# Performance work log

Measured on AMD Instinct MI355X. Metric: run time of the kernel, lower is better.

Reference implementation:

```python
import jax, jax.numpy as jnp
import numpy as np

N = 50000   # nodes
E = 800000  # edges
F = 128     # input features
W = 128     # hidden width
K = 5       # Chebyshev order


def setup_inputs() -> dict:
    key = jax.random.key(0)
    ks = jax.random.split(key, 12)
    x = jax.random.normal(ks[0], (N, F), jnp.float32)
    edge_index = jax.random.randint(ks[1], (2, E), 0, N, jnp.int32)
    def p(i, shape):
        return jax.random.normal(ks[i], shape, jnp.float32) * 0.05
    return {
        'x': x,
        'edge_index': edge_index,
        'W0': p(2, (K, F, W)), 'b0': p(3, (W,)),
        'W1': p(4, (K, W, W)), 'b1': p(5, (W,)),
        'W2': p(6, (K, W, W)), 'b2': p(7, (W,)),
        'Wl': p(8, (W, 1)),   'bl': p(9, (1,)),
    }


def _norm(edge_index):
    # PyG ChebConv norm with lambda_max=2.0, sym normalization:
    # Lhat = 2/lambda_max * (I - D^-1/2 A D^-1/2) - I  ->  diag 0, offdiag -d_r*d_c
    src, dst = edge_index[0], edge_index[1]
    ew = (src != dst).astype(jnp.float32)  # remove self loops
    deg = jax.ops.segment_sum(ew, src, num_segments=N)
    dinv = jnp.where(deg > 0, jax.lax.rsqrt(jnp.maximum(deg, 1.0)), 0.0)
    w = -ew * dinv[src] * dinv[dst]
    return src, dst, w


def _cheb_conv(h, Wk, b, src, dst, w):
    # Tx_0 = h; Tx_1 = Lhat h; Tx_k = 2 Lhat Tx_{k-1} - Tx_{k-2}
    def matvec(v):
        # gather from src, weight, scatter-add to dst: [E, C] message tensor
        return jax.ops.segment_sum(w[:, None] * v[src], dst, num_segments=N)
    Tx0 = h
    out = Tx0 @ Wk[0]
    Tx1 = matvec(Tx0)
    out = out + Tx1 @ Wk[1]
    for k in range(2, Wk.shape[0]):
        Tx2 = 2.0 * matvec(Tx1) - Tx0
        out = out + Tx2 @ Wk[k]
        Tx0, Tx1 = Tx1, Tx2
    return out + b


def reference(x, edge_index, W0, b0, W1, b1, W2, b2, Wl, bl):
    src, dst, w = _norm(edge_index)
    h = jax.nn.relu(_cheb_conv(x, W0, b0, src, dst, w))  # dropout = identity (eval)
    h = jax.nn.relu(_cheb_conv(h, W1, b1, src, dst, w))
    h = _cheb_conv(h, W2, b2, src, dst, w)
    return h @ Wl + bl  # [N, 1]
```

## Files before the change

kernel.cpp:

```cpp
#include <hip/hip_runtime.h>
#include <hip/hip_bf16.h>
#include <stdint.h>

#define N_NODES 50000
#define N_EDGES 800000
#define FEAT 128
#define CAP 64
#define NCVT 1600000

#define B_CONV 6250
#define B_TRW  640
#define B_EDGE 3125
#define B_TOT  10018

typedef __attribute__((ext_vector_type(4))) float floatx4;
typedef __attribute__((ext_vector_type(8))) _Float16 half8;
typedef __attribute__((ext_vector_type(4))) _Float16 half4;
typedef __attribute__((ext_vector_type(4))) unsigned short ushortx4;

__device__ __forceinline__ float bf2f(unsigned short u) {
  union { unsigned u; float f; } v; v.u = ((unsigned)u) << 16; return v.f;
}
__device__ __forceinline__ unsigned short f2bf(float f) {
  union { float f; unsigned u; } v; v.f = f;
  unsigned r = v.u + 0x7fffu + ((v.u >> 16) & 1u);
  return (unsigned short)(r >> 16);
}
__device__ __forceinline__ unsigned pack_edge(float w, int s) {
  _Float16 h = (_Float16)w;
  unsigned short hb = __builtin_bit_cast(unsigned short, h);
  return ((unsigned)s << 16) | (unsigned)hb;
}
__device__ __forceinline__ float edge_w(unsigned e) {
  unsigned short hb = (unsigned short)(e & 0xFFFFu);
  return (float)__builtin_bit_cast(_Float16, hb);
}
__device__ __forceinline__ int edge_src(unsigned e) { return (int)(e >> 16); }

__global__ void k_pre1(const unsigned short* __restrict__ x,
                       const void* b0, const void* b1, const void* b2,
                       const void* wl, const void* bl,
                       float* __restrict__ pf, int* __restrict__ flag) {
  __shared__ int cnt_s;
  __shared__ int fl_s;
  int tid = threadIdx.x;
  if (tid == 0) cnt_s = 0;
  __syncthreads();
  int big = 0;
  for (int i = tid; i < 4096; i += 256) {
    unsigned short u = x[2 * i];
    int e = (u >> 7) & 0xFF;
    if (e >= 0xE0) big++;
  }
  atomicAdd(&cnt_s, big);
  __syncthreads();
  if (tid == 0) { fl_s = (cnt_s > 16) ? 1 : 0; flag[0] = fl_s; }
  __syncthreads();
  int fl = fl_s;
  for (int i = tid; i < 513; i += 256) {
    const void* src; int off;
    if (i < 128)      { src = b0; off = i; }
    else if (i < 256) { src = b1; off = i - 128; }
    else if (i < 384) { src = b2; off = i - 256; }
    else if (i < 512) { src = wl; off = i - 384; }
    else              { src = bl; off = 0; }
    pf[i] = fl ? ((const float*)src)[off] : bf2f(((const unsigned short*)src)[off]);
  }
}

__global__ void k_pre2(const void* __restrict__ xp,
                       const void* __restrict__ w0, const void* __restrict__ w1,
                       const void* __restrict__ w2,
                       const int* __restrict__ esrc, const int* __restrict__ edst,
                       _Float16* __restrict__ t0,
                       unsigned char* __restrict__ q0, float* __restrict__ s0,
                       _Float16* __restrict__ wt,
                       int* __restrict__ deg, int* __restrict__ cnt,
                       unsigned short* __restrict__ edata16,
                       float* __restrict__ pf,
                       const int* __restrict__ flag) {
  int b = blockIdx.x, tid = threadIdx.x;
  int o;
  if (b < 10000) {
    int g = b >> 4, r = b & 15;
    if (r < 5) {
      int e = (g * 5 + r) * 256 + tid;
      int s = __builtin_nontemporal_load(esrc + e);
      int d = __builtin_nontemporal_load(edst + e);
      if (s == d) return;
      atomicAdd(&deg[s], 1);
      int pos = atomicAdd(&cnt[d], 1);
      if (pos < CAP) edata16[((size_t)d << 6) + pos] = (unsigned short)s;
      return;
    }
    o = g * 11 + (r - 5);
  } else {
    o = 6875 + (b - 10000);
  }
  if (o < B_CONV) {
    int i = o * 256 + tid;
    int fl = flag[0];
    floatx4 v;
    if (fl) {
      v = __builtin_nontemporal_load((const floatx4*)xp + i);
    } else {
      ushortx4 u = __builtin_nontemporal_load((const ushortx4*)xp + i);
      v.x = bf2f(u.x); v.y = bf2f(u.y); v.z = bf2f(u.z); v.w = bf2f(u.w);
    }
    half4 h;
    h[0] = (_Float16)v.x; h[1] = (_Float16)v.y; h[2] = (_Float16)v.z; h[3] = (_Float16)v.w;
    ((half4*)t0)[i] = h;
    float mx = fmaxf(fmaxf(fabsf(v.x), fabsf(v.y)), fmaxf(fabsf(v.z), fabsf(v.w)));
#pragma unroll
    for (int d = 1; d < 32; d <<= 1) mx = fmaxf(mx, __shfl_xor(mx, d));
    float inv = mx > 0.f ? 127.f / mx : 0.f;
    int qa = (int)rintf(v.x * inv) + 128;
    int qb = (int)rintf(v.y * inv) + 128;
    int qc = (int)rintf(v.z * inv) + 128;
    int qd = (int)rintf(v.w * inv) + 128;
    ((unsigned*)q0)[i] = (unsigned)qa | ((unsigned)qb << 8) | ((unsigned)qc << 16) | ((unsigned)qd << 24);
    if ((i & 31) == 0) s0[i >> 5] = mx > 0.f ? mx / 127.f : 0.f;
  } else if (o < B_CONV + B_TRW) {
    int t = (o - B_CONV) * 256 + tid;
    int fl = flag[0];
    int li = t >> 14;
    int r = t & 16383;
    int n = r >> 7, kk = r & 127;
    int l = li / 5, k = li - l * 5;
    const void* w = (l == 0) ? w0 : w1;
    int idx = k * 16384 + kk * 128 + n;
    float v = fl ? ((const float*)w)[idx] : bf2f(((const unsigned short*)w)[idx]);
    wt[t] = (_Float16)v;
  } else {
    int t = (o - B_CONV - B_TRW) * 256 + tid;
    if (t > 640) return;
    int fl = flag[0];
    if (t < 640) {
      int k = t >> 7, f = t & 127;
      float s = 0.f;
      const int base = (k << 14) + (f << 7);
      if (fl) {
        const float* w = (const float*)w2 + base;
#pragma unroll 8
        for (int q = 0; q < 128; ++q) s += w[q] * pf[384 + q];
      } else {
        const unsigned short* w = (const unsigned short*)w2 + base;
#pragma unroll 8
        for (int q = 0; q < 128; ++q) s += bf2f(w[q]) * pf[384 + q];
      }
      pf[520 + t] = s;
    } else {
      float s = 0.f;
      for (int q = 0; q < 128; ++q) s += pf[256 + q] * pf[384 + q];
      pf[1160] = s + pf[512];
    }
  }
}

__global__ __launch_bounds__(256) void k_wpack(const unsigned short* __restrict__ ed16,
                                               const int* __restrict__ cnt,
                                               const int* __restrict__ deg,
                                               unsigned* __restrict__ edata) {
  int t = blockIdx.x * 256 + threadIdx.x;
  int node = t >> 6, slot = t & 63;
  if (node >= N_NODES) return;
  int n_e = cnt[node]; if (n_e > CAP) n_e = CAP;
  unsigned out = 0u;
  if (slot < n_e) {
    int s = (int)ed16[t];
    int dd = deg[node];
    int ds = deg[s];
    float w = (ds > 0 && dd > 0) ? -rsqrtf((float)ds) * rsqrtf((float)dd) : 0.f;
    out = pack_edge(w, s);
  }
  edata[t] = out;
}

__global__ __launch_bounds__(256) void k_spmv(const unsigned* __restrict__ edata,
                                              const int* __restrict__ cnt,
                                              const unsigned char* __restrict__ Q,
                                              const float* __restrict__ S,
                                              const _Float16* __restrict__ Z,
                                              _Float16* __restrict__ Y,
                                              unsigned char* __restrict__ Qo,
                                              float* __restrict__ So,
                                              float alpha, int hasZ, int wshadow) {
  int wave = threadIdx.x >> 6, lane = threadIdx.x & 63;
  int q = lane >> 4, l16 = lane & 15;
  int node = blockIdx.x * 16 + wave * 4 + q;
  if (node >= N_NODES) return;
  int n_e = cnt[node]; if (n_e > CAP) n_e = CAP;
  int base = node << 6;

  float acc[8];
#pragma unroll
  for (int f = 0; f < 8; ++f) acc[f] = 0.f;
  float wsum = 0.f;

  unsigned e0 = (0 < n_e) ? edata[base + 0] : 0u;
  unsigned e1 = (1 < n_e) ? edata[base + 1] : 0u;
  unsigned e2 = (2 < n_e) ? edata[base + 2] : 0u;
  unsigned e3 = (3 < n_e) ? edata[base + 3] : 0u;
  unsigned e4 = (4 < n_e) ? edata[base + 4] : 0u;
  unsigned e5 = (5 < n_e) ? edata[base + 5] : 0u;
  unsigned e6 = (6 < n_e) ? edata[base + 6] : 0u;
  unsigned e7 = (7 < n_e) ? edata[base + 7] : 0u;
  uint2 r0 = ((const uint2*)(Q + (size_t)edge_src(e0) * FEAT))[l16];
  uint2 r1 = ((const uint2*)(Q + (size_t)edge_src(e1) * FEAT))[l16];
  uint2 r2 = ((const uint2*)(Q + (size_t)edge_src(e2) * FEAT))[l16];
  uint2 r3 = ((const uint2*)(Q + (size_t)edge_src(e3) * FEAT))[l16];
  float s0 = S[edge_src(e0)], s1 = S[edge_src(e1)], s2 = S[edge_src(e2)], s3 = S[edge_src(e3)];

  for (int j = 0; j < n_e; j += 4) {
    float ws0 = edge_w(e0) * s0, ws1 = edge_w(e1) * s1;
    float ws2 = edge_w(e2) * s2, ws3 = edge_w(e3) * s3;
    uint2 c0 = r0, c1 = r1, c2 = r2, c3 = r3;
    e0 = e4; e1 = e5; e2 = e6; e3 = e7;
    e4 = (j + 8 < n_e) ? edata[base + j + 8] : 0u;
    e5 = (j + 9 < n_e) ? edata[base + j + 9] : 0u;
    e6 = (j + 10 < n_e) ? edata[base + j + 10] : 0u;
    e7 = (j + 11 < n_e) ? edata[base + j + 11] : 0u;
    r0 = ((const uint2*)(Q + (size_t)edge_src(e0) * FEAT))[l16];
    r1 = ((const uint2*)(Q + (size_t)edge_src(e1) * FEAT))[l16];
    r2 = ((const uint2*)(Q + (size_t)edge_src(e2) * FEAT))[l16];
    r3 = ((const uint2*)(Q + (size_t)edge_src(e3) * FEAT))[l16];
    s0 = S[edge_src(e0)]; s1 = S[edge_src(e1)]; s2 = S[edge_src(e2)]; s3 = S[edge_src(e3)];
#define DEC8(c, w)                                                        \
    acc[0] = fmaf(w, (float)(c.x & 0xFFu), acc[0]);                       \
    acc[1] = fmaf(w, (float)((c.x >> 8) & 0xFFu), acc[1]);                \
    acc[2] = fmaf(w, (float)((c.x >> 16) & 0xFFu), acc[2]);               \
    acc[3] = fmaf(w, (float)(c.x >> 24), acc[3]);                         \
    acc[4] = fmaf(w, (float)(c.y & 0xFFu), acc[4]);                       \
    acc[5] = fmaf(w, (float)((c.y >> 8) & 0xFFu), acc[5]);                \
    acc[6] = fmaf(w, (float)((c.y >> 16) & 0xFFu), acc[6]);               \
    acc[7] = fmaf(w, (float)(c.y >> 24), acc[7]);
    DEC8(c0, ws0) DEC8(c1, ws1) DEC8(c2, ws2) DEC8(c3, ws3)
#undef DEC8
    wsum += (ws0 + ws1) + (ws2 + ws3);
  }
  float rx[8];
  float b128 = 128.f * wsum;
  if (hasZ) {
    half8 z = ((const half8*)(Z + (size_t)node * FEAT))[l16];
#pragma unroll
    for (int f = 0; f < 8; ++f) rx[f] = fmaf(alpha, acc[f] - b128, -(float)z[f]);
  } else {
#pragma unroll
    for (int f = 0; f < 8; ++f) rx[f] = alpha * (acc[f] - b128);
  }
  half8 res;
#pragma unroll
  for (int f = 0; f < 8; ++f) res[f] = (_Float16)rx[f];
  ((half8*)(Y + (size_t)node * FEAT))[l16] = res;
  if (wshadow) {
    float mx = 0.f;
#pragma unroll
    for (int f = 0; f < 8; ++f) mx = fmaxf(mx, fabsf(rx[f]));
#pragma unroll
    for (int o = 1; o < 16; o <<= 1) mx = fmaxf(mx, __shfl_xor(mx, o));
    float inv = mx > 0.f ? 127.f / mx : 0.f;
    int qb[8];
#pragma unroll
    for (int f = 0; f < 8; ++f) qb[f] = (int)rintf(rx[f] * inv) + 128;
    uint2 p;
    p.x = (unsigned)qb[0] | ((unsigned)qb[1] << 8) | ((unsigned)qb[2] << 16) | ((unsigned)qb[3] << 24);
    p.y = (unsigned)qb[4] | ((unsigned)qb[5] << 8) | ((unsigned)qb[6] << 16) | ((unsigned)qb[7] << 24);
    ((uint2*)(Qo + (size_t)node * FEAT))[l16] = p;
    if (l16 == 0) So[node] = mx > 0.f ? mx / 127.f : 0.f;
  }
}

__global__ __launch_bounds__(256) void k_smv(const unsigned* __restrict__ edata,
                                             const int* __restrict__ cnt,
                                             const float* __restrict__ h,
                                             const float* __restrict__ b,
                                             const float* __restrict__ bprev,
                                             float cL, float* __restrict__ y,
                                             int is_out, void* __restrict__ outp,
                                             const int* __restrict__ flag,
                                             const float* __restrict__ cptr) {
  int wave = threadIdx.x >> 6, lane = threadIdx.x & 63;
  int q = lane >> 4, l16 = lane & 15;
  int node = blockIdx.x * 16 + wave * 4 + q;
  if (node >= N_NODES) return;
  int n_e = cnt[node]; if (n_e > CAP) n_e = CAP;
  int base = node << 6;
  float s = 0.f;
  for (int j = l16; j < n_e; j += 16) {
    unsigned e = edata[base + j];
    s = fmaf(edge_w(e), b[edge_src(e)], s);
  }
#pragma unroll
  for (int o = 1; o < 16; o <<= 1) s += __shfl_xor(s, o);
  if (l16 == 0) {
    float r = fmaf(cL, s, h[node]) - (bprev ? bprev[node] : 0.f);
    if (!is_out) {
      y[node] = r;
    } else {
      r += cptr[0];
      if (flag[0]) ((float*)outp)[node] = r;
      else ((unsigned short*)outp)[node] = f2bf(r);
    }
  }
}

__global__ __launch_bounds__(256) void k_gemm(const _Float16* __restrict__ t0, const _Float16* __restrict__ t1,
                                              const _Float16* __restrict__ t2, const _Float16* __restrict__ t3,
                                              const _Float16* __restrict__ t4,
                                              const _Float16* __restrict__ wt,
                                              const float* __restrict__ bias,
                                              _Float16* __restrict__ dst, int mode,
                                              const float* __restrict__ v0,
                                              float* __restrict__ hout,
                                              unsigned char* __restrict__ q8,
                                              float* __restrict__ sc) {
  __shared__ _Float16 lb[128 * 136];
  const _Float16* tp[5] = {t0, t1, t2, t3, t4};
  int tid = threadIdx.x, wave = tid >> 6, lane = tid & 63;
  int quad = lane >> 4, l16 = lane & 15;
  int m0 = blockIdx.x * 128;
  floatx4 acc[2][8];
#pragma unroll
  for (int s = 0; s < 2; ++s)
#pragma unroll
    for (int j = 0; j < 8; ++j) acc[s][j] = (floatx4){0.f, 0.f, 0.f, 0.f};
  int arow[2];
  bool aval[2];
#pragma unroll
  for (int s = 0; s < 2; ++s) {
    arow[s] = m0 + wave * 32 + s * 16 + l16;
    aval[s] = arow[s] < N_NODES;
  }

#pragma unroll
  for (int k = 0; k < 5; ++k) {
    __syncthreads();
    {
      int n = tid >> 1, half = tid & 1;
      const uint4* sp = (const uint4*)(wt + k * 16384 + n * 128 + half * 64);
      uint4* dq = (uint4*)(lb + n * 136 + half * 64);
#pragma unroll
      for (int i = 0; i < 8; ++i) dq[i] = sp[i];
    }
    __syncthreads();
    const _Float16* A = tp[k];
#pragma unroll
    for (int ki = 0; ki < 4; ++ki) {
      half8 af[2];
#pragma unroll
      for (int s = 0; s < 2; ++s) {
        if (aval[s]) {
          af[s] = *((const half8*)(A + (size_t)arow[s] * FEAT + ki * 32 + quad * 8));
        } else {
#pragma unroll
          for (int i = 0; i < 8; ++i) af[s][i] = (_Float16)0.f;
        }
      }
#pragma unroll
      for (int j = 0; j < 8; ++j) {
        half8 bf = *((const half8*)(lb + (j * 16 + l16) * 136 + ki * 32 + quad * 8));
        acc[0][j] = __builtin_amdgcn_mfma_f32_16x16x32_f16(af[0], bf, acc[0][j], 0, 0, 0);
        acc[1][j] = __builtin_amdgcn_mfma_f32_16x16x32_f16(af[1], bf, acc[1][j], 0, 0, 0);
      }
    }
  }
#pragma unroll
  for (int s = 0; s < 2; ++s) {
    int rbase = m0 + wave * 32 + s * 16 + quad * 4;
    if (mode == 0) {
      float mx[4] = {0.f, 0.f, 0.f, 0.f};
#pragma unroll
      for (int j = 0; j < 8; ++j) {
        int col = j * 16 + l16;
        float b = bias[col];
#pragma unroll
        for (int r = 0; r < 4; ++r) {
          int m = rbase + r;
          float v = fmaxf(acc[s][j][r] + b, 0.f);
          if (m < N_NODES) dst[(size_t)m * FEAT + col] = (_Float16)v;
          mx[r] = fmaxf(mx[r], v);
        }
      }
#pragma unroll
      for (int o = 1; o < 16; o <<= 1) {
#pragma unroll
        for (int r = 0; r < 4; ++r) mx[r] = fmaxf(mx[r], __shfl_xor(mx[r], o));
      }
      float inv[4];
#pragma unroll
      for (int r = 0; r < 4; ++r) inv[r] = mx[r] > 0.f ? 127.f / mx[r] : 0.f;
      if (l16 == 0) {
#pragma unroll
        for (int r = 0; r < 4; ++r) {
          int m = rbase + r;
          if (m < N_NODES) sc[m] = mx[r] > 0.f ? mx[r] / 127.f : 0.f;
        }
      }
#pragma unroll
      for (int j = 0; j < 8; ++j) {
        int col = j * 16 + l16;
        float b = bias[col];
#pragma unroll
        for (int r = 0; r < 4; ++r) {
          int m = rbase + r;
          if (m < N_NODES) {
            float v = fmaxf(acc[s][j][r] + b, 0.f);
            int qv = (int)rintf(v * inv[r]) + 128;
            q8[(size_t)m * FEAT + col] = (unsigned char)qv;
          }
        }
      }
    } else {
      float p[5][4];
#pragma unroll
      for (int k = 0; k < 5; ++k)
#pragma unroll
        for (int r = 0; r < 4; ++r) p[k][r] = 0.f;
#pragma unroll
      for (int j = 0; j < 8; ++j) {
        int col = j * 16 + l16;
        float b = bias[col];
        float vv[5];
#pragma unroll
        for (int k = 0; k < 5; ++k) vv[k] = v0[k * 128 + col];
#pragma unroll
        for (int r = 0; r < 4; ++r) {
          float val = fmaxf(acc[s][j][r] + b, 0.f);
#pragma unroll
          for (int k = 0; k < 5; ++k) p[k][r] = fmaf(val, vv[k], p[k][r]);
        }
      }
#pragma unroll
      for (int o = 1; o < 16; o <<= 1) {
#pragma unroll
        for (int k = 0; k < 5; ++k)
#pragma unroll
          for (int r = 0; r < 4; ++r) p[k][r] += __shfl_xor(p[k][r], o);
      }
      if (l16 == 0) {
#pragma unroll
        for (int r = 0; r < 4; ++r) {
          int m = rbase + r;
          if (m < N_NODES) {
#pragma unroll
            for (int k = 0; k < 5; ++k) hout[k * N_NODES + m] = p[k][r];
          }
        }
      }
    }
  }
}

extern "C" void kernel_launch(void* const* d_in, const int* in_sizes, int n_in,
                              void* d_out, int out_size, void* d_ws, size_t ws_size,
                              hipStream_t stream) {
  const void* x  = d_in[0];
  const int* ei  = (const int*)d_in[1];
  const void* w0 = d_in[2];
  const void* b0 = d_in[3];
  const void* w1 = d_in[4];
  const void* b1 = d_in[5];
  const void* w2 = d_in[6];
  const void* b2 = d_in[7];
  const void* wl = d_in[8];
  const void* bl = d_in[9];
  const int* src = ei;
  const int* dst = ei + N_EDGES;

  char* ws = (char*)d_ws;
  size_t off = 0;
  auto alloc = [&](size_t bytes) -> char* {
    char* p = ws + off;
    off += (bytes + 255) & ~(size_t)255;
    return p;
  };
  _Float16* T[5];
  for (int i = 0; i < 5; ++i) T[i] = (_Float16*)alloc(sizeof(_Float16) * N_NODES * FEAT);
  unsigned char* Q[5];
  for (int i = 0; i < 5; ++i) Q[i] = (unsigned char*)alloc((size_t)N_NODES * FEAT);
  float* S[5];
  for (int i = 0; i < 5; ++i) S[i] = (float*)alloc(sizeof(float) * N_NODES);
  unsigned* edata = (unsigned*)alloc(sizeof(unsigned) * N_NODES * CAP);
  unsigned short* edata16 = (unsigned short*)alloc(sizeof(unsigned short) * N_NODES * CAP);
  int* cnt = (int*)alloc(sizeof(int) * N_NODES * 2);
  int* deg = cnt + N_NODES;
  _Float16* wt = (_Float16*)alloc(sizeof(_Float16) * 163840);
  float* pf = (float*)alloc(sizeof(float) * 1536);
  float* hbuf = (float*)alloc(sizeof(float) * 5 * N_NODES);
  float* bbuf = (float*)alloc(sizeof(float) * 3 * N_NODES);
  int* flag = (int*)alloc(sizeof(int));

  hipMemsetAsync(cnt, 0, sizeof(int) * N_NODES * 2, stream);
  k_pre1<<<1, 256, 0, stream>>>((const unsigned short*)x, b0, b1, b2, wl, bl, pf, flag);
  k_pre2<<<B_TOT, 256, 0, stream>>>(x, w0, w1, w2, src, dst, T[0], Q[0], S[0], wt,
                                    deg, cnt, edata16, pf, flag);
  k_wpack<<<(N_NODES * CAP) / 256, 256, 0, stream>>>(edata16, cnt, deg, edata);

  int nblk_spmv = (N_NODES + 15) / 16;
  int nblk_gemm = (N_NODES + 127) / 128;
  const float* v = pf + 520;
  const float* cc = pf + 1160;

  for (int l = 0; l < 2; ++l) {
    k_spmv<<<nblk_spmv, 256, 0, stream>>>(edata, cnt, Q[0], S[0], nullptr, T[1], Q[1], S[1], 1.f, 0, 1);
    k_spmv<<<nblk_spmv, 256, 0, stream>>>(edata, cnt, Q[1], S[1], T[0], T[2], Q[2], S[2], 2.f, 1, 1);
    k_spmv<<<nblk_spmv, 256, 0, stream>>>(edata, cnt, Q[2], S[2], T[1], T[3], Q[3], S[3], 2.f, 1, 1);
    k_spmv<<<nblk_spmv, 256, 0, stream>>>(edata, cnt, Q[3], S[3], T[2], T[4], nullptr, nullptr, 2.f, 1, 0);
    k_gemm<<<nblk_gemm, 256, 0, stream>>>(T[0], T[1], T[2], T[3], T[4],
                                          wt + l * 5 * 16384, pf + l * 128, T[0],
                                          l, v, hbuf, Q[0], S[0]);
  }
  float* h0 = hbuf;
  float* h1 = hbuf + N_NODES;
  float* h2 = hbuf + 2 * N_NODES;
  float* h3 = hbuf + 3 * N_NODES;
  float* h4 = hbuf + 4 * N_NODES;
  float* b3 = bbuf;
  float* b2c = bbuf + N_NODES;
  float* b1c = bbuf + 2 * N_NODES;
  k_smv<<<nblk_spmv, 256, 0, stream>>>(edata, cnt, h3, h4, nullptr, 2.f, b3, 0, nullptr, flag, nullptr);
  k_smv<<<nblk_spmv, 256, 0, stream>>>(edata, cnt, h2, b3, h4, 2.f, b2c, 0, nullptr, flag, nullptr);
  k_smv<<<nblk_spmv, 256, 0, stream>>>(edata, cnt, h1, b2c, b3, 2.f, b1c, 0, nullptr, flag, nullptr);
  k_smv<<<nblk_spmv, 256, 0, stream>>>(edata, cnt, h0, b1c, b2c, 1.f, nullptr, 1, d_out, flag, cc);
}
```

Before: 455.8 us.

## Feed GEMM from int8 shadow copies and partition edge bucketing atomics

The Chebyshev GEMM now reads the int8-quantized Tx_k buffers with per-row scales and dequantizes them in registers, instead of reading fp16 copies. The last two SpMV passes therefore skip writing fp16 outputs and only emit int8 plus scale, which cuts both write and read traffic. Edge bucketing spreads the per-destination counter atomics over 8 partitions with 16 slots each, and the pack kernel compacts them into a single 64-slot list per node, easing atomic contention. The cost is extra rounding error in GEMM inputs, and a node whose edges fall unevenly across partitions can drop edges once one partition passes 16.

After: 456.7 us. About the same (+0.2%).

```diff
diff --git a/kernel.cpp b/kernel.cpp
--- a/kernel.cpp
+++ b/kernel.cpp
@@ -6,11 +6,11 @@
 #define N_EDGES 800000
 #define FEAT 128
 #define CAP 64
+#define PSLOT 16
 #define NCVT 1600000
 
 #define B_CONV 6250
 #define B_TRW  640
-#define B_EDGE 3125
 #define B_TOT  10018
 
 typedef __attribute__((ext_vector_type(4))) float floatx4;
@@ -36,6 +36,19 @@
   return (float)__builtin_bit_cast(_Float16, hb);
 }
 __device__ __forceinline__ int edge_src(unsigned e) { return (int)(e >> 16); }
+
+__device__ __forceinline__ half8 deq8(uint2 v, float sc) {
+  half8 r;
+  r[0] = (_Float16)(sc * (float)((int)(v.x & 0xFFu) - 128));
+  r[1] = (_Float16)(sc * (float)((int)((v.x >> 8) & 0xFFu) - 128));
+  r[2] = (_Float16)(sc * (float)((int)((v.x >> 16) & 0xFFu) - 128));
+  r[3] = (_Float16)(sc * (float)((int)(v.x >> 24) - 128));
+  r[4] = (_Float16)(sc * (float)((int)(v.y & 0xFFu) - 128));
+  r[5] = (_Float16)(sc * (float)((int)((v.y >> 8) & 0xFFu) - 128));
+  r[6] = (_Float16)(sc * (float)((int)((v.y >> 16) & 0xFFu) - 128));
+  r[7] = (_Float16)(sc * (float)((int)(v.y >> 24) - 128));
+  return r;
+}
 
 __global__ void k_pre1(const unsigned short* __restrict__ x,
                        const void* b0, const void* b1, const void* b2,
@@ -75,7 +88,7 @@
                        _Float16* __restrict__ t0,
                        unsigned char* __restrict__ q0, float* __restrict__ s0,
                        _Float16* __restrict__ wt,
-                       int* __restrict__ deg, int* __restrict__ cnt,
+                       int* __restrict__ deg, int* __restrict__ cnt8,
                        unsigned short* __restrict__ edata16,
                        float* __restrict__ pf,
                        const int* __restrict__ flag) {
@@ -84,13 +97,15 @@
   if (b < 10000) {
     int g = b >> 4, r = b & 15;
     if (r < 5) {
+      int p = b & 7;
       int e = (g * 5 + r) * 256 + tid;
       int s = __builtin_nontemporal_load(esrc + e);
       int d = __builtin_nontemporal_load(edst + e);
       if (s == d) return;
       atomicAdd(&deg[s], 1);
-      int pos = atomicAdd(&cnt[d], 1);
-      if (pos < CAP) edata16[((size_t)d << 6) + pos] = (unsigned short)s;
+      int pos = atomicAdd(&cnt8[p * N_NODES + d], 1);
+      if (pos < PSLOT)
+        edata16[(size_t)p * (N_NODES * PSLOT) + d * PSLOT + pos] = (unsigned short)s;
       return;
     }
     o = g * 11 + (r - 5);
@@ -158,22 +173,37 @@
 }
 
 __global__ __launch_bounds__(256) void k_wpack(const unsigned short* __restrict__ ed16,
-                                               const int* __restrict__ cnt,
+                                               const int* __restrict__ cnt8,
                                                const int* __restrict__ deg,
+                                               int* __restrict__ cnt,
                                                unsigned* __restrict__ edata) {
-  int t = blockIdx.x * 256 + threadIdx.x;
-  int node = t >> 6, slot = t & 63;
+  int node = (blockIdx.x * 256 + threadIdx.x) >> 6;
+  int lane = threadIdx.x & 63;
   if (node >= N_NODES) return;
-  int n_e = cnt[node]; if (n_e > CAP) n_e = CAP;
-  unsigned out = 0u;
-  if (slot < n_e) {
-    int s = (int)ed16[t];
-    int dd = deg[node];
-    int ds = deg[s];
-    float w = (ds > 0 && dd > 0) ? -rsqrtf((float)ds) * rsqrtf((float)dd) : 0.f;
-    out = pack_edge(w, s);
-  }
-  edata[t] = out;
+  int c[8], off[8], tot = 0;
+#pragma unroll
+  for (int p = 0; p < 8; ++p) {
+    int v = cnt8[p * N_NODES + node];
+    if (v > PSLOT) v = PSLOT;
+    c[p] = v; off[p] = tot; tot += v;
+  }
+  if (lane == 0) cnt[node] = tot > CAP ? CAP : tot;
+  int dd = deg[node];
+  float rd = dd > 0 ? rsqrtf((float)dd) : 0.f;
+#pragma unroll
+  for (int it = 0; it < 2; ++it) {
+    int p = (lane >> 4) + it * 4;
+    int s = lane & 15;
+    if (s < c[p]) {
+      int pos = off[p] + s;
+      if (pos < CAP) {
+        int sr = (int)ed16[(size_t)p * (N_NODES * PSLOT) + node * PSLOT + s];
+        int ds = deg[sr];
+        float w = (ds > 0 && dd > 0) ? -rsqrtf((float)ds) * rd : 0.f;
+        edata[(node << 6) + pos] = pack_edge(w, sr);
+      }
+    }
+  }
 }
 
 __global__ __launch_bounds__(256) void k_spmv(const unsigned* __restrict__ edata,
@@ -184,7 +214,7 @@
                                               _Float16* __restrict__ Y,
                                               unsigned char* __restrict__ Qo,
                                               float* __restrict__ So,
-                                              float alpha, int hasZ, int wshadow) {
+                                              float alpha, int hasZ, int writeY) {
   int wave = threadIdx.x >> 6, lane = threadIdx.x & 63;
   int q = lane >> 4, l16 = lane & 15;
   int node = blockIdx.x * 16 + wave * 4 + q;
@@ -248,26 +278,26 @@
 #pragma unroll
     for (int f = 0; f < 8; ++f) rx[f] = alpha * (acc[f] - b128);
   }
-  half8 res;
-#pragma unroll
-  for (int f = 0; f < 8; ++f) res[f] = (_Float16)rx[f];
-  ((half8*)(Y + (size_t)node * FEAT))[l16] = res;
-  if (wshadow) {
-    float mx = 0.f;
-#pragma unroll
-    for (int f = 0; f < 8; ++f) mx = fmaxf(mx, fabsf(rx[f]));
-#pragma unroll
-    for (int o = 1; o < 16; o <<= 1) mx = fmaxf(mx, __shfl_xor(mx, o));
-    float inv = mx > 0.f ? 127.f / mx : 0.f;
-    int qb[8];
-#pragma unroll
-    for (int f = 0; f < 8; ++f) qb[f] = (int)rintf(rx[f] * inv) + 128;
-    uint2 p;
-    p.x = (unsigned)qb[0] | ((unsigned)qb[1] << 8) | ((unsigned)qb[2] << 16) | ((unsigned)qb[3] << 24);
-    p.y = (unsigned)qb[4] | ((unsigned)qb[5] << 8) | ((unsigned)qb[6] << 16) | ((unsigned)qb[7] << 24);
-    ((uint2*)(Qo + (size_t)node * FEAT))[l16] = p;
-    if (l16 == 0) So[node] = mx > 0.f ? mx / 127.f : 0.f;
-  }
+  if (writeY) {
+    half8 res;
+#pragma unroll
+    for (int f = 0; f < 8; ++f) res[f] = (_Float16)rx[f];
+    ((half8*)(Y + (size_t)node * FEAT))[l16] = res;
+  }
+  float mx = 0.f;
+#pragma unroll
+  for (int f = 0; f < 8; ++f) mx = fmaxf(mx, fabsf(rx[f]));
+#pragma unroll
+  for (int o = 1; o < 16; o <<= 1) mx = fmaxf(mx, __shfl_xor(mx, o));
+  float inv = mx > 0.f ? 127.f / mx : 0.f;
+  int qb[8];
+#pragma unroll
+  for (int f = 0; f < 8; ++f) qb[f] = (int)rintf(rx[f] * inv) + 128;
+  uint2 p;
+  p.x = (unsigned)qb[0] | ((unsigned)qb[1] << 8) | ((unsigned)qb[2] << 16) | ((unsigned)qb[3] << 24);
+  p.y = (unsigned)qb[4] | ((unsigned)qb[5] << 8) | ((unsigned)qb[6] << 16) | ((unsigned)qb[7] << 24);
+  ((uint2*)(Qo + (size_t)node * FEAT))[l16] = p;
+  if (l16 == 0) So[node] = mx > 0.f ? mx / 127.f : 0.f;
 }
 
 __global__ __launch_bounds__(256) void k_smv(const unsigned* __restrict__ edata,
@@ -304,18 +334,22 @@
   }
 }
 
-__global__ __launch_bounds__(256) void k_gemm(const _Float16* __restrict__ t0, const _Float16* __restrict__ t1,
-                                              const _Float16* __restrict__ t2, const _Float16* __restrict__ t3,
-                                              const _Float16* __restrict__ t4,
+__global__ __launch_bounds__(256) void k_gemm(const unsigned char* __restrict__ qa0, const unsigned char* __restrict__ qa1,
+                                              const unsigned char* __restrict__ qa2, const unsigned char* __restrict__ qa3,
+                                              const unsigned char* __restrict__ qa4,
+                                              const float* __restrict__ sa0, const float* __restrict__ sa1,
+                                              const float* __restrict__ sa2, const float* __restrict__ sa3,
+                                              const float* __restrict__ sa4,
                                               const _Float16* __restrict__ wt,
                                               const float* __restrict__ bias,
                                               _Float16* __restrict__ dst, int mode,
                                               const float* __restrict__ v0,
                                               float* __restrict__ hout,
-                                              unsigned char* __restrict__ q8,
-                                              float* __restrict__ sc) {
+                                              unsigned char* __restrict__ q8out,
+                                              float* __restrict__ scout) {
   __shared__ _Float16 lb[128 * 136];
-  const _Float16* tp[5] = {t0, t1, t2, t3, t4};
+  const unsigned char* qp[5] = {qa0, qa1, qa2, qa3, qa4};
+  const float* sp[5] = {sa0, sa1, sa2, sa3, sa4};
   int tid = threadIdx.x, wave = tid >> 6, lane = tid & 63;
   int quad = lane >> 4, l16 = lane & 15;
   int m0 = blockIdx.x * 128;
@@ -337,24 +371,25 @@
     __syncthreads();
     {
       int n = tid >> 1, half = tid & 1;
-      const uint4* sp = (const uint4*)(wt + k * 16384 + n * 128 + half * 64);
+      const uint4* spw = (const uint4*)(wt + k * 16384 + n * 128 + half * 64);
       uint4* dq = (uint4*)(lb + n * 136 + half * 64);
 #pragma unroll
-      for (int i = 0; i < 8; ++i) dq[i] = sp[i];
+      for (int i = 0; i < 8; ++i) dq[i] = spw[i];
     }
     __syncthreads();
-    const _Float16* A = tp[k];
+    const unsigned char* Aq = qp[k];
+    float sk[2];
+#pragma unroll
+    for (int s = 0; s < 2; ++s) sk[s] = aval[s] ? sp[k][arow[s]] : 0.f;
 #pragma unroll
     for (int ki = 0; ki < 4; ++ki) {
       half8 af[2];
 #pragma unroll
       for (int s = 0; s < 2; ++s) {
-        if (aval[s]) {
-          af[s] = *((const half8*)(A + (size_t)arow[s] * FEAT + ki * 32 + quad * 8));
-        } else {
-#pragma unroll
-          for (int i = 0; i < 8; ++i) af[s][i] = (_Float16)0.f;
-        }
+        uint2 qv = aval[s]
+          ? *((const uint2*)(Aq + (size_t)arow[s] * FEAT + ki * 32 + quad * 8))
+          : make_uint2(0x80808080u, 0x80808080u);
+        af[s] = deq8(qv, sk[s]);
       }
 #pragma unroll
       for (int j = 0; j < 8; ++j) {
@@ -393,7 +428,7 @@
 #pragma unroll
         for (int r = 0; r < 4; ++r) {
           int m = rbase + r;
-          if (m < N_NODES) sc[m] = mx[r] > 0.f ? mx[r] / 127.f : 0.f;
+          if (m < N_NODES) scout[m] = mx[r] > 0.f ? mx[r] / 127.f : 0.f;
         }
       }
 #pragma unroll
@@ -406,7 +441,7 @@
           if (m < N_NODES) {
             float v = fmaxf(acc[s][j][r] + b, 0.f);
             int qv = (int)rintf(v * inv[r]) + 128;
-            q8[(size_t)m * FEAT + col] = (unsigned char)qv;
+            q8out[(size_t)m * FEAT + col] = (unsigned char)qv;
           }
         }
       }
@@ -474,27 +509,28 @@
     off += (bytes + 255) & ~(size_t)255;
     return p;
   };
-  _Float16* T[5];
-  for (int i = 0; i < 5; ++i) T[i] = (_Float16*)alloc(sizeof(_Float16) * N_NODES * FEAT);
+  _Float16* T[3];
+  for (int i = 0; i < 3; ++i) T[i] = (_Float16*)alloc(sizeof(_Float16) * N_NODES * FEAT);
   unsigned char* Q[5];
   for (int i = 0; i < 5; ++i) Q[i] = (unsigned char*)alloc((size_t)N_NODES * FEAT);
   float* S[5];
   for (int i = 0; i < 5; ++i) S[i] = (float*)alloc(sizeof(float) * N_NODES);
   unsigned* edata = (unsigned*)alloc(sizeof(unsigned) * N_NODES * CAP);
-  unsigned short* edata16 = (unsigned short*)alloc(sizeof(unsigned short) * N_NODES * CAP);
-  int* cnt = (int*)alloc(sizeof(int) * N_NODES * 2);
-  int* deg = cnt + N_NODES;
+  unsigned short* edata16 = (unsigned short*)alloc(sizeof(unsigned short) * 8 * N_NODES * PSLOT);
+  int* cnt8 = (int*)alloc(sizeof(int) * N_NODES * 9);
+  int* deg = cnt8 + 8 * N_NODES;
+  int* cnt = (int*)alloc(sizeof(int) * N_NODES);
   _Float16* wt = (_Float16*)alloc(sizeof(_Float16) * 163840);
   float* pf = (float*)alloc(sizeof(float) * 1536);
   float* hbuf = (float*)alloc(sizeof(float) * 5 * N_NODES);
   float* bbuf = (float*)alloc(sizeof(float) * 3 * N_NODES);
   int* flag = (int*)alloc(sizeof(int));
 
-  hipMemsetAsync(cnt, 0, sizeof(int) * N_NODES * 2, stream);
+  hipMemsetAsync(cnt8, 0, sizeof(int) * N_NODES * 9, stream);
   k_pre1<<<1, 256, 0, stream>>>((const unsigned short*)x, b0, b1, b2, wl, bl, pf, flag);
   k_pre2<<<B_TOT, 256, 0, stream>>>(x, w0, w1, w2, src, dst, T[0], Q[0], S[0], wt,
-                                    deg, cnt, edata16, pf, flag);
-  k_wpack<<<(N_NODES * CAP) / 256, 256, 0, stream>>>(edata16, cnt, deg, edata);
+                                    deg, cnt8, edata16, pf, flag);
+  k_wpack<<<(N_NODES * 64 + 255) / 256, 256, 0, stream>>>(edata16, cnt8, deg, cnt, edata);
 
   int nblk_spmv = (N_NODES + 15) / 16;
   int nblk_gemm = (N_NODES + 127) / 128;
@@ -504,9 +540,10 @@
   for (int l = 0; l < 2; ++l) {
     k_spmv<<<nblk_spmv, 256, 0, stream>>>(edata, cnt, Q[0], S[0], nullptr, T[1], Q[1], S[1], 1.f, 0, 1);
     k_spmv<<<nblk_spmv, 256, 0, stream>>>(edata, cnt, Q[1], S[1], T[0], T[2], Q[2], S[2], 2.f, 1, 1);
-    k_spmv<<<nblk_spmv, 256, 0, stream>>>(edata, cnt, Q[2], S[2], T[1], T[3], Q[3], S[3], 2.f, 1, 1);
-    k_spmv<<<nblk_spmv, 256, 0, stream>>>(edata, cnt, Q[3], S[3], T[2], T[4], nullptr, nullptr, 2.f, 1, 0);
-    k_gemm<<<nblk_gemm, 256, 0, stream>>>(T[0], T[1], T[2], T[3], T[4],
+    k_spmv<<<nblk_spmv, 256, 0, stream>>>(edata, cnt, Q[2], S[2], T[1], nullptr, Q[3], S[3], 2.f, 1, 0);
+    k_spmv<<<nblk_spmv, 256, 0, stream>>>(edata, cnt, Q[3], S[3], T[2], nullptr, Q[4], S[4], 2.f, 1, 0);
+    k_gemm<<<nblk_gemm, 256, 0, stream>>>(Q[0], Q[1], Q[2], Q[3], Q[4],
+                                          S[0], S[1], S[2], S[3], S[4],
                                           wt + l * 5 * 16384, pf + l * 128, T[0],
                                           l, v, hbuf, Q[0], S[0]);
   }
```
